# Optimization experiments

Measured on AMD Instinct MI355X. Metric: run time of the kernel, lower is better.

## Reference

```python
import jax, jax.numpy as jnp
import numpy as np

D_MODEL = 1024
NUM_HEADS = 16
HEAD_DIM = D_MODEL // NUM_HEADS
D_FF = 4096
BATCH = 4
SEQ = 2048
LN_EPS = 1e-6
NEG_INF = -1e10


def setup_inputs() -> dict:
    key = jax.random.key(0)
    ks = jax.random.split(key, 8)
    def lin_init(k, fan_in, fan_out):
        # flax default: lecun_normal kernel, zeros bias
        w = jax.random.normal(k, (fan_in, fan_out), jnp.float32) / np.sqrt(fan_in)
        b = jnp.zeros((fan_out,), jnp.float32)
        return w, b
    x = jax.random.normal(ks[0], (BATCH, SEQ, D_MODEL), jnp.float32)
    w_qkv, b_qkv = lin_init(ks[1], D_MODEL, 3 * D_MODEL)
    w_out, b_out = lin_init(ks[2], D_MODEL, D_MODEL)
    w_fc1, b_fc1 = lin_init(ks[3], D_MODEL, D_FF)
    w_fc2, b_fc2 = lin_init(ks[4], D_FF, D_MODEL)
    ln1_scale = jnp.ones((D_MODEL,), jnp.float32)
    ln1_bias = jnp.zeros((D_MODEL,), jnp.float32)
    ln2_scale = jnp.ones((D_MODEL,), jnp.float32)
    ln2_bias = jnp.zeros((D_MODEL,), jnp.float32)
    return {
        'x': x,
        'w_qkv': w_qkv, 'b_qkv': b_qkv,
        'w_out': w_out, 'b_out': b_out,
        'w_fc1': w_fc1, 'b_fc1': b_fc1,
        'w_fc2': w_fc2, 'b_fc2': b_fc2,
        'ln1_scale': ln1_scale, 'ln1_bias': ln1_bias,
        'ln2_scale': ln2_scale, 'ln2_bias': ln2_bias,
    }


def _layernorm(x, scale, bias):
    mu = jnp.mean(x, axis=-1, keepdims=True)
    var = jnp.mean(jnp.square(x - mu), axis=-1, keepdims=True)
    return (x - mu) * jax.lax.rsqrt(var + LN_EPS) * scale + bias


def _attention(x, w_qkv, b_qkv, w_out, b_out):
    B, S, _ = x.shape
    qkv = x @ w_qkv + b_qkv                      # [B,S,3*D]
    qkv = qkv.reshape(B, S, 3, NUM_HEADS, HEAD_DIM)
    q, k, v = qkv[:, :, 0], qkv[:, :, 1], qkv[:, :, 2]   # [B,S,H,D]
    q = q.transpose(0, 2, 1, 3)                  # [B,H,S,D]
    k = k.transpose(0, 2, 1, 3)
    v = v.transpose(0, 2, 1, 3)
    scores = jnp.einsum('bhqd,bhkd->bhqk', q, k) / np.sqrt(HEAD_DIM)
    causal = jnp.tril(jnp.ones((S, S), bool))[None, None]
    scores = jnp.where(causal, scores, NEG_INF)
    attn = jax.nn.softmax(scores, axis=-1)
    out = jnp.einsum('bhqk,bhkd->bhqd', attn, v)  # [B,H,S,D]
    out = out.transpose(0, 2, 1, 3).reshape(B, S, D_MODEL)
    return out @ w_out + b_out


def _mlp(x, w_fc1, b_fc1, w_fc2, b_fc2):
    h = jax.nn.gelu(x @ w_fc1 + b_fc1)  # approximate (tanh) gelu, matching nnx.gelu default
    return h @ w_fc2 + b_fc2


def reference(x, w_qkv, b_qkv, w_out, b_out, w_fc1, b_fc1, w_fc2, b_fc2,
              ln1_scale, ln1_bias, ln2_scale, ln2_bias):
    x = x + _attention(_layernorm(x, ln1_scale, ln1_bias), w_qkv, b_qkv, w_out, b_out)
    x = x + _mlp(_layernorm(x, ln2_scale, ln2_bias), w_fc1, b_fc1, w_fc2, b_fc2)
    return x
```

## Files before the change

kernel.cpp:

```cpp
#include <hip/hip_runtime.h>

typedef unsigned short u16;
typedef unsigned int u32;
typedef __bf16 bf16x8 __attribute__((ext_vector_type(8)));
typedef float f32x4 __attribute__((ext_vector_type(4)));

constexpr int SEQ = 2048;

__device__ __forceinline__ float bf2f(u16 u) {
    u32 x = ((u32)u) << 16;
    return __builtin_bit_cast(float, x);
}
__device__ __forceinline__ u16 f2bf(float f) {
    u32 u = __builtin_bit_cast(u32, f);
    u32 r = u + 0x7fffu + ((u >> 16) & 1u);
    return (u16)(r >> 16);
}
__device__ __forceinline__ bf16x8 ld_frag(const u16* p) {
    uint4 u = *(const uint4*)p;
    return __builtin_bit_cast(bf16x8, u);
}
__device__ __forceinline__ float gelu_f(float x) {
    float u = 0.7978845608028654f * (x + 0.044715f * x * x * x);
    float e = exp2f(u * 2.885390081777927f);
    float t = 1.f - 2.f / (1.f + e);
    return 0.5f * x * (1.f + t);
}
__device__ __forceinline__ bool probe_f32(const u32* p) { return (p[0] & 0xFFFFu) == 0u; }

__device__ __forceinline__ void load_lds16(const u16* g, u16* l) {
    __builtin_amdgcn_global_load_lds(
        (const __attribute__((address_space(1))) void*)g,
        (__attribute__((address_space(3))) void*)l, 16, 0, 0);
}

__global__ __launch_bounds__(256) void convert_to_bf16(const void* __restrict__ in, long long off,
                                                       u16* __restrict__ out, int n,
                                                       const u32* __restrict__ probe) {
    const bool f32 = probe_f32(probe);
    int i = (blockIdx.x * 256 + threadIdx.x) * 4;
    if (i >= n) return;
    if (f32) {
        const float4 v = *(const float4*)((const float*)in + off + i);
        uint2 o;
        o.x = (u32)f2bf(v.x) | ((u32)f2bf(v.y) << 16);
        o.y = (u32)f2bf(v.z) | ((u32)f2bf(v.w) << 16);
        *(uint2*)(out + i) = o;
    } else {
        *(uint2*)(out + i) = *(const uint2*)((const u16*)in + off + i);
    }
}

__global__ __launch_bounds__(256) void finalize_out(const u16* __restrict__ in, void* __restrict__ outv,
                                                    long long off, int n, const u32* __restrict__ probe) {
    const bool f32 = probe_f32(probe);
    int i = (blockIdx.x * 256 + threadIdx.x) * 4;
    if (i >= n) return;
    uint2 v = *(const uint2*)(in + i);
    if (f32) {
        float4 o;
        o.x = bf2f((u16)(v.x & 0xffffu));
        o.y = bf2f((u16)(v.x >> 16));
        o.z = bf2f((u16)(v.y & 0xffffu));
        o.w = bf2f((u16)(v.y >> 16));
        *(float4*)((float*)outv + off + i) = o;
    } else {
        *(uint2*)((u16*)outv + off + i) = v;
    }
}

__global__ __launch_bounds__(256) void transpose_any(const void* __restrict__ in,
                                                     u16* __restrict__ out,
                                                     int K, int N, const u32* __restrict__ probe) {
    const bool f32 = probe_f32(probe);
    __shared__ u16 tile[32][33];
    int tx = threadIdx.x & 31, ty = threadIdx.x >> 5;
    int k0 = blockIdx.y * 32, n0 = blockIdx.x * 32;
    for (int i = 0; i < 32; i += 8) {
        size_t idx = (size_t)(k0 + ty + i) * N + n0 + tx;
        tile[ty + i][tx] = f32 ? f2bf(((const float*)in)[idx]) : ((const u16*)in)[idx];
    }
    __syncthreads();
    for (int i = 0; i < 32; i += 8)
        out[(size_t)(n0 + ty + i) * K + k0 + tx] = tile[tx][ty + i];
}

__global__ __launch_bounds__(256) void layernorm_k(const u16* __restrict__ x,
                                                   const u16* __restrict__ sc,
                                                   const u16* __restrict__ bi,
                                                   u16* __restrict__ out) {
    int row = blockIdx.x;
    int tid = threadIdx.x;
    const u16* xr = x + (size_t)row * 1024;
    uint2 u = *(const uint2*)(xr + tid * 4);
    float v[4];
    v[0] = bf2f((u16)(u.x & 0xffffu));
    v[1] = bf2f((u16)(u.x >> 16));
    v[2] = bf2f((u16)(u.y & 0xffffu));
    v[3] = bf2f((u16)(u.y >> 16));
    float s1 = 0.f, s2 = 0.f;
    for (int i = 0; i < 4; i++) { s1 += v[i]; s2 += v[i] * v[i]; }
    for (int off = 32; off >= 1; off >>= 1) {
        s1 += __shfl_xor(s1, off, 64);
        s2 += __shfl_xor(s2, off, 64);
    }
    __shared__ float red[8];
    int wave = tid >> 6, lane = tid & 63;
    if (lane == 0) { red[wave] = s1; red[4 + wave] = s2; }
    __syncthreads();
    s1 = red[0] + red[1] + red[2] + red[3];
    s2 = red[4] + red[5] + red[6] + red[7];
    float mean = s1 * (1.f / 1024.f);
    float var = s2 * (1.f / 1024.f) - mean * mean;
    float rstd = rsqrtf(var + 1e-6f);
    u32 o0, o1;
    {
        int c = tid * 4;
        float y0 = (v[0] - mean) * rstd * bf2f(sc[c + 0]) + bf2f(bi[c + 0]);
        float y1 = (v[1] - mean) * rstd * bf2f(sc[c + 1]) + bf2f(bi[c + 1]);
        float y2 = (v[2] - mean) * rstd * bf2f(sc[c + 2]) + bf2f(bi[c + 2]);
        float y3 = (v[3] - mean) * rstd * bf2f(sc[c + 3]) + bf2f(bi[c + 3]);
        o0 = (u32)f2bf(y0) | ((u32)f2bf(y1) << 16);
        o1 = (u32)f2bf(y2) | ((u32)f2bf(y3) << 16);
    }
    uint2 ov; ov.x = o0; ov.y = o1;
    *(uint2*)(out + (size_t)row * 1024 + tid * 4) = ov;
}

__device__ __forceinline__ void gemm_core(const u16* __restrict__ A, const u16* __restrict__ Bt,
                                          int K, int bm, int bn,
                                          u16* lA, u16* lB, f32x4 acc[4][4]) {
    const int tid = threadIdx.x, lane = tid & 63, wave = tid >> 6;
    const int wr = (wave >> 1) * 64, wc = (wave & 1) * 64;
    const int g = lane >> 4, l15 = lane & 15;
    const int srow = wave * 32 + (lane >> 3);
    const int scol = (lane & 7) * 8;
    const u16* gA = A + (size_t)(bm + srow) * K + scol;
    const u16* gB = Bt + (size_t)(bn + srow) * K + scol;
    u16* lAb = lA + wave * 2048;
    u16* lBb = lB + wave * 2048;

    for (int kk = 0; kk < K; kk += 64) {
        __syncthreads();
#pragma unroll
        for (int q = 0; q < 4; q++) {
            load_lds16(gA + kk + q * 8 * K, lAb + q * 512);
            load_lds16(gB + kk + q * 8 * K, lBb + q * 512);
        }
        __syncthreads();
#pragma unroll
        for (int kh = 0; kh < 2; kh++) {
            bf16x8 af[4], bfr[4];
#pragma unroll
            for (int i = 0; i < 4; i++)
                af[i] = ld_frag(lA + (wr + i * 16 + l15) * 64 + (kh * 4 + g) * 8);
#pragma unroll
            for (int j = 0; j < 4; j++)
                bfr[j] = ld_frag(lB + (wc + j * 16 + l15) * 64 + (kh * 4 + g) * 8);
#pragma unroll
            for (int i = 0; i < 4; i++)
#pragma unroll
                for (int j = 0; j < 4; j++)
                    acc[i][j] = __builtin_amdgcn_mfma_f32_16x16x32_bf16(bfr[j], af[i], acc[i][j], 0, 0, 0);
        }
    }
}

__global__ __launch_bounds__(256) void gemm_bt(const u16* __restrict__ A,
                                               const u16* __restrict__ Bt,
                                               const u16* __restrict__ bias,
                                               const u16* __restrict__ res,
                                               u16* __restrict__ out,
                                               int M, int N, int K, int epi) {
    __shared__ __align__(16) u16 lA[128 * 64];
    __shared__ __align__(16) u16 lB[128 * 64];
    const int tid = threadIdx.x, lane = tid & 63, wave = tid >> 6;
    const int wr = (wave >> 1) * 64, wc = (wave & 1) * 64;
    const int g = lane >> 4, l15 = lane & 15;
    const int bm = blockIdx.y * 128, bn = blockIdx.x * 128;

    f32x4 acc[4][4];
    f32x4 zero = {0.f, 0.f, 0.f, 0.f};
    for (int i = 0; i < 4; i++)
        for (int j = 0; j < 4; j++) acc[i][j] = zero;

    gemm_core(A, Bt, K, bm, bn, lA, lB, acc);

    for (int j = 0; j < 4; j++) {
        const int gn0 = bn + wc + j * 16 + g * 4;
        const uint2 bv2 = *(const uint2*)(bias + gn0);
        const float b0 = bf2f((u16)(bv2.x & 0xffffu)), b1 = bf2f((u16)(bv2.x >> 16));
        const float b2 = bf2f((u16)(bv2.y & 0xffffu)), b3 = bf2f((u16)(bv2.y >> 16));
        for (int i = 0; i < 4; i++) {
            const int gm = bm + wr + i * 16 + l15;
            float v0 = acc[i][j][0] + b0, v1 = acc[i][j][1] + b1;
            float v2 = acc[i][j][2] + b2, v3 = acc[i][j][3] + b3;
            if (epi == 1) {
                const uint2 rv = *(const uint2*)(res + (size_t)gm * N + gn0);
                v0 += bf2f((u16)(rv.x & 0xffffu)); v1 += bf2f((u16)(rv.x >> 16));
                v2 += bf2f((u16)(rv.y & 0xffffu)); v3 += bf2f((u16)(rv.y >> 16));
            } else if (epi == 2) {
                v0 = gelu_f(v0); v1 = gelu_f(v1); v2 = gelu_f(v2); v3 = gelu_f(v3);
            }
            ushort4 o4;
            o4.x = f2bf(v0); o4.y = f2bf(v1); o4.z = f2bf(v2); o4.w = f2bf(v3);
            *(ushort4*)(out + (size_t)gm * N + gn0) = o4;
        }
    }
}

__global__ __launch_bounds__(256) void gemm_qkv(const u16* __restrict__ A,
                                                const u16* __restrict__ Bt,
                                                const u16* __restrict__ bias,
                                                u16* __restrict__ Qg,
                                                u16* __restrict__ Kg,
                                                u16* __restrict__ VTg,
                                                int K) {
    __shared__ __align__(16) u16 lA[128 * 64];
    __shared__ __align__(16) u16 lB[128 * 64];
    const int tid = threadIdx.x, lane = tid & 63, wave = tid >> 6;
    const int wr = (wave >> 1) * 64, wc = (wave & 1) * 64;
    const int g = lane >> 4, l15 = lane & 15;
    const int bm = blockIdx.y * 128, bn = blockIdx.x * 128;
    const float QSCALE = 0.18033688011112042f;

    f32x4 acc[4][4];
    f32x4 zero = {0.f, 0.f, 0.f, 0.f};
    for (int i = 0; i < 4; i++)
        for (int j = 0; j < 4; j++) acc[i][j] = zero;

    gemm_core(A, Bt, K, bm, bn, lA, lB, acc);

    for (int j = 0; j < 4; j++) {
        const int gn0 = bn + wc + j * 16 + g * 4;
        const int which = gn0 >> 10;
        const int hh = (gn0 >> 6) & 15, d0 = gn0 & 63;
        const uint2 bv2 = *(const uint2*)(bias + gn0);
        const float b0 = bf2f((u16)(bv2.x & 0xffffu)), b1 = bf2f((u16)(bv2.x >> 16));
        const float b2 = bf2f((u16)(bv2.y & 0xffffu)), b3 = bf2f((u16)(bv2.y >> 16));
        for (int i = 0; i < 4; i++) {
            const int s0 = bm + wr + i * 16 + l15;
            const int b = s0 >> 11, srel = s0 & 2047;
            const int bh = b * 16 + hh;
            const float v0 = acc[i][j][0] + b0, v1 = acc[i][j][1] + b1;
            const float v2 = acc[i][j][2] + b2, v3 = acc[i][j][3] + b3;
            if (which == 0) {
                ushort4 o4;
                o4.x = f2bf(v0 * QSCALE); o4.y = f2bf(v1 * QSCALE);
                o4.z = f2bf(v2 * QSCALE); o4.w = f2bf(v3 * QSCALE);
                *(ushort4*)(Qg + ((size_t)bh * SEQ + srel) * 64 + d0) = o4;
            } else if (which == 1) {
                ushort4 o4;
                o4.x = f2bf(v0); o4.y = f2bf(v1); o4.z = f2bf(v2); o4.w = f2bf(v3);
                *(ushort4*)(Kg + ((size_t)bh * SEQ + srel) * 64 + d0) = o4;
            } else {
                VTg[((size_t)bh * 64 + d0 + 0) * SEQ + srel] = f2bf(v0);
                VTg[((size_t)bh * 64 + d0 + 1) * SEQ + srel] = f2bf(v1);
                VTg[((size_t)bh * 64 + d0 + 2) * SEQ + srel] = f2bf(v2);
                VTg[((size_t)bh * 64 + d0 + 3) * SEQ + srel] = f2bf(v3);
            }
        }
    }
}

__device__ __forceinline__ void stage_kv(const u16* Kbh, const u16* Vbh, int kv0,
                                         u16* bK, u16* bV, int lane, int wave) {
    const int r = lane >> 3, c = (lane & 7) * 8;
#pragma unroll
    for (int q = 0; q < 2; q++) {
        const int row = q * 32 + wave * 8 + r;
        load_lds16(Kbh + (size_t)(kv0 + row) * 64 + c, bK + q * 2048 + wave * 512 + lane * 8);
        load_lds16(Vbh + (size_t)row * SEQ + kv0 + c, bV + q * 2048 + wave * 512 + lane * 8);
    }
}

__global__ __launch_bounds__(256) void flash_attn5(const u16* __restrict__ Qg,
                                                   const u16* __restrict__ Kg,
                                                   const u16* __restrict__ VTg,
                                                   u16* __restrict__ attn) {
    __shared__ __align__(16) u16 lK[2][64 * 64];
    __shared__ __align__(16) u16 lVt[2][64 * 64];
    __shared__ __align__(16) u16 lP[4 * 32 * 72];

    const int bh = blockIdx.y;
    const int tid = threadIdx.x, lane = tid & 63, wave = tid >> 6;
    const int g = lane >> 4, l15 = lane & 15;
    const float MASKV = -3.0e4f;

    const u16* Qbh = Qg + (size_t)bh * SEQ * 64;
    const u16* Kbh = Kg + (size_t)bh * SEQ * 64;
    const u16* Vbh = VTg + (size_t)bh * 64 * SEQ;
    u16* myP = lP + wave * 32 * 72;
    const int b = bh >> 4, h = bh & 15;
    const f32x4 zero = {0.f, 0.f, 0.f, 0.f};

    for (int ph = 0; ph < 2; ph++) {
        const int ti = ph ? blockIdx.x : (15 - blockIdx.x);
        const int q0 = ti * 128;
        const int qw = q0 + wave * 32;
        const int nfull = q0 >> 6;
        const int nt = nfull + 2;

        bf16x8 qf[2][2];
#pragma unroll
        for (int mi = 0; mi < 2; mi++)
#pragma unroll
            for (int kh = 0; kh < 2; kh++)
                qf[mi][kh] = ld_frag(Qbh + (size_t)(qw + mi * 16 + l15) * 64 + kh * 32 + g * 8);

        float l_[2][4];
        f32x4 o[2][4];
        for (int mi = 0; mi < 2; mi++)
            for (int r = 0; r < 4; r++) l_[mi][r] = 0.f;
        for (int mi = 0; mi < 2; mi++)
            for (int nj = 0; nj < 4; nj++) o[mi][nj] = zero;

        __syncthreads();
        stage_kv(Kbh, Vbh, 0, lK[0], lVt[0], lane, wave);

        for (int t = 0; t < nt; t++) {
            __syncthreads();
            if (t + 1 < nt)
                stage_kv(Kbh, Vbh, (t + 1) * 64, lK[(t + 1) & 1], lVt[(t + 1) & 1], lane, wave);
            const u16* bK = lK[t & 1];
            const u16* bV = lVt[t & 1];
            const bool diag = (t >= nfull);
            const int kv0 = t * 64;

            f32x4 sc[2][4];
#pragma unroll
            for (int mi = 0; mi < 2; mi++)
                for (int nj = 0; nj < 4; nj++) sc[mi][nj] = zero;
#pragma unroll
            for (int kh = 0; kh < 2; kh++) {
                bf16x8 kf[4];
#pragma unroll
                for (int nj = 0; nj < 4; nj++)
                    kf[nj] = ld_frag(bK + (nj * 16 + l15) * 64 + kh * 32 + g * 8);
#pragma unroll
                for (int mi = 0; mi < 2; mi++)
#pragma unroll
                    for (int nj = 0; nj < 4; nj++)
                        sc[mi][nj] = __builtin_amdgcn_mfma_f32_16x16x32_bf16(qf[mi][kh], kf[nj], sc[mi][nj], 0, 0, 0);
            }

#pragma unroll
            for (int mi = 0; mi < 2; mi++) {
#pragma unroll
                for (int r = 0; r < 4; r++) {
                    const int row = qw + mi * 16 + g * 4 + r;
                    float v0 = sc[mi][0][r], v1 = sc[mi][1][r];
                    float v2 = sc[mi][2][r], v3 = sc[mi][3][r];
                    if (diag) {
                        if (kv0 + 0 * 16 + l15 > row) v0 = MASKV;
                        if (kv0 + 1 * 16 + l15 > row) v1 = MASKV;
                        if (kv0 + 2 * 16 + l15 > row) v2 = MASKV;
                        if (kv0 + 3 * 16 + l15 > row) v3 = MASKV;
                    }
                    const float e0 = exp2f(v0), e1 = exp2f(v1);
                    const float e2 = exp2f(v2), e3 = exp2f(v3);
                    l_[mi][r] += (e0 + e1) + (e2 + e3);
                    const int prow = (mi * 16 + g * 4 + r) * 72;
                    myP[prow + 0 * 16 + l15] = f2bf(e0);
                    myP[prow + 1 * 16 + l15] = f2bf(e1);
                    myP[prow + 2 * 16 + l15] = f2bf(e2);
                    myP[prow + 3 * 16 + l15] = f2bf(e3);
                }
            }

#pragma unroll
            for (int ks = 0; ks < 2; ks++) {
                bf16x8 pa[2], vb[4];
#pragma unroll
                for (int mi = 0; mi < 2; mi++)
                    pa[mi] = ld_frag(myP + (mi * 16 + l15) * 72 + ks * 32 + g * 8);
#pragma unroll
                for (int nj = 0; nj < 4; nj++)
                    vb[nj] = ld_frag(bV + (nj * 16 + l15) * 64 + ks * 32 + g * 8);
#pragma unroll
                for (int mi = 0; mi < 2; mi++)
#pragma unroll
                    for (int nj = 0; nj < 4; nj++)
                        o[mi][nj] = __builtin_amdgcn_mfma_f32_16x16x32_bf16(pa[mi], vb[nj], o[mi][nj], 0, 0, 0);
            }
        }

#pragma unroll
        for (int mi = 0; mi < 2; mi++) {
            for (int r = 0; r < 4; r++) {
                float ls = l_[mi][r];
                for (int off = 1; off < 16; off <<= 1) ls += __shfl_xor(ls, off, 64);
                const float inv = 1.f / ls;
                const int row = qw + mi * 16 + g * 4 + r;
                const size_t orow = ((size_t)b * SEQ + row) * 1024 + h * 64;
                for (int nj = 0; nj < 4; nj++)
                    attn[orow + nj * 16 + l15] = f2bf(o[mi][nj][r] * inv);
            }
        }
    }
}

extern "C" void kernel_launch(void* const* d_in, const int* in_sizes, int n_in,
                              void* d_out, int out_size, void* d_ws, size_t ws_size,
                              hipStream_t stream) {
    const u32* probe = (const u32*)d_in[9];
    char* ws = (char*)d_ws;
    const size_t MB = 1048576;
    auto T = [&](size_t mb) { return (u16*)(ws + mb * MB); };
    auto conv = [&](const void* src, long long off, u16* dst, int n) {
        convert_to_bf16<<<(n / 4 + 255) / 256, 256, 0, stream>>>(src, off, dst, n, probe);
    };

    if (ws_size >= 160 * MB) {
        u16* xn1 = T(0), *Qg = T(16), *Kg = T(32), *VTg = T(48), *hbuf = T(0);
        u16* attn = T(64), *xn2 = T(64), *xbf = T(80), *resid1 = T(96), *outbf = T(112);
        u16* wTq = T(128), *wTo = T(134), *wT1 = T(136), *wT2 = T(144), *vecs = T(152);
        u16 *bqkvC = vecs, *boutC = vecs + 3072, *bfc1C = vecs + 4096, *bfc2C = vecs + 8192;
        u16 *ln1sC = vecs + 9216, *ln1bC = vecs + 10240, *ln2sC = vecs + 11264, *ln2bC = vecs + 12288;
        conv(d_in[2], 0, bqkvC, 3072); conv(d_in[4], 0, boutC, 1024);
        conv(d_in[6], 0, bfc1C, 4096); conv(d_in[8], 0, bfc2C, 1024);
        conv(d_in[9], 0, ln1sC, 1024); conv(d_in[10], 0, ln1bC, 1024);
        conv(d_in[11], 0, ln2sC, 1024); conv(d_in[12], 0, ln2bC, 1024);
        transpose_any<<<dim3(96, 32), 256, 0, stream>>>(d_in[1], wTq, 1024, 3072, probe);
        transpose_any<<<dim3(32, 32), 256, 0, stream>>>(d_in[3], wTo, 1024, 1024, probe);
        transpose_any<<<dim3(128, 32), 256, 0, stream>>>(d_in[5], wT1, 1024, 4096, probe);
        transpose_any<<<dim3(32, 128), 256, 0, stream>>>(d_in[7], wT2, 4096, 1024, probe);
        conv(d_in[0], 0, xbf, 8388608);
        layernorm_k<<<8192, 256, 0, stream>>>(xbf, ln1sC, ln1bC, xn1);
        gemm_qkv<<<dim3(24, 64), 256, 0, stream>>>(xn1, wTq, bqkvC, Qg, Kg, VTg, 1024);
        flash_attn5<<<dim3(8, 64), 256, 0, stream>>>(Qg, Kg, VTg, attn);
        gemm_bt<<<dim3(8, 64), 256, 0, stream>>>(attn, wTo, boutC, xbf, resid1, 8192, 1024, 1024, 1);
        layernorm_k<<<8192, 256, 0, stream>>>(resid1, ln2sC, ln2bC, xn2);
        gemm_bt<<<dim3(32, 64), 256, 0, stream>>>(xn2, wT1, bfc1C, nullptr, hbuf, 8192, 4096, 1024, 2);
        gemm_bt<<<dim3(8, 64), 256, 0, stream>>>(hbuf, wT2, bfc2C, resid1, outbf, 8192, 1024, 4096, 1);
        finalize_out<<<8192, 256, 0, stream>>>(outbf, d_out, 0, 8388608, probe);
    } else {
        u16* vecs = T(0);
        u16 *bqkvC = vecs, *boutC = vecs + 3072, *bfc1C = vecs + 4096, *bfc2C = vecs + 8192;
        u16 *ln1sC = vecs + 9216, *ln1bC = vecs + 10240, *ln2sC = vecs + 11264, *ln2bC = vecs + 12288;
        u16* wTq = T(1), *wTo = T(7), *wT1 = T(9), *wT2 = T(17);
        u16* xbf = T(25), *xn = T(29), *Qg = T(33), *Kg = T(37), *VTg = T(41);
        u16* attn_b = T(45), *resid_b = T(49), *h_b = T(53);
        conv(d_in[2], 0, bqkvC, 3072); conv(d_in[4], 0, boutC, 1024);
        conv(d_in[6], 0, bfc1C, 4096); conv(d_in[8], 0, bfc2C, 1024);
        conv(d_in[9], 0, ln1sC, 1024); conv(d_in[10], 0, ln1bC, 1024);
        conv(d_in[11], 0, ln2sC, 1024); conv(d_in[12], 0, ln2bC, 1024);
        transpose_any<<<dim3(96, 32), 256, 0, stream>>>(d_in[1], wTq, 1024, 3072, probe);
        transpose_any<<<dim3(32, 32), 256, 0, stream>>>(d_in[3], wTo, 1024, 1024, probe);
        transpose_any<<<dim3(128, 32), 256, 0, stream>>>(d_in[5], wT1, 1024, 4096, probe);
        transpose_any<<<dim3(32, 128), 256, 0, stream>>>(d_in[7], wT2, 4096, 1024, probe);
        for (int b = 0; b < 4; b++) {
            const long long ro = (long long)b * 2048 * 1024;
            conv(d_in[0], ro, xbf, 2097152);
            layernorm_k<<<2048, 256, 0, stream>>>(xbf, ln1sC, ln1bC, xn);
            gemm_qkv<<<dim3(24, 16), 256, 0, stream>>>(xn, wTq, bqkvC, Qg, Kg, VTg, 1024);
            flash_attn5<<<dim3(8, 16), 256, 0, stream>>>(Qg, Kg, VTg, attn_b);
            gemm_bt<<<dim3(8, 16), 256, 0, stream>>>(attn_b, wTo, boutC, xbf, resid_b, 2048, 1024, 1024, 1);
            layernorm_k<<<2048, 256, 0, stream>>>(resid_b, ln2sC, ln2bC, xn);
            for (int c = 0; c < 2; c++) {
                u16* xnc = xn + (size_t)c * 1024 * 1024;
                u16* resc = resid_b + (size_t)c * 1024 * 1024;
                u16* outc = xbf + (size_t)c * 1024 * 1024;
                gemm_bt<<<dim3(32, 8), 256, 0, stream>>>(xnc, wT1, bfc1C, nullptr, h_b, 1024, 4096, 1024, 2);
                gemm_bt<<<dim3(8, 8), 256, 0, stream>>>(h_b, wT2, bfc2C, resc, outc, 1024, 1024, 4096, 1);
                finalize_out<<<1024, 256, 0, stream>>>(outc, d_out, ro + c * 1048576, 1048576, probe);
            }
        }
    }
}
```

Measured before the change: 636.6 us.

## XOR-swizzle LDS tiles in GEMM and flash attention; fuse input convert with LayerNorm

Global-to-LDS loads now place each 16-byte chunk at a slot XORed with the row index, and fragment reads apply the matching XOR. This affects the GEMM core and the K/V staging in flash attention and is meant to remove LDS bank conflicts on the 64-wide bf16 rows. Separately, the input fp32-to-bf16 conversion and the first LayerNorm are merged into one kernel that writes both the bf16 copy and the normalized output, saving one pass over x. The swizzle has to match exactly between writer and reader; the visible hunks look consistent, but any other consumer of the same LDS buffers that was not updated would read wrong data.

```diff
diff --git a/kernel.cpp b/kernel.cpp
--- a/kernel.cpp
+++ b/kernel.cpp
@@ -83,6 +83,56 @@
     __syncthreads();
     for (int i = 0; i < 32; i += 8)
         out[(size_t)(n0 + ty + i) * K + k0 + tx] = tile[tx][ty + i];
+}
+
+__global__ __launch_bounds__(256) void fused_cvt_ln(const void* __restrict__ xraw, long long off,
+                                                    const u16* __restrict__ sc,
+                                                    const u16* __restrict__ bi,
+                                                    u16* __restrict__ xbf,
+                                                    u16* __restrict__ xn,
+                                                    const u32* __restrict__ probe) {
+    const bool f32 = probe_f32(probe);
+    int row = blockIdx.x;
+    int tid = threadIdx.x;
+    float v[4];
+    if (f32) {
+        const float4 q = *(const float4*)((const float*)xraw + off + (size_t)row * 1024 + tid * 4);
+        v[0] = q.x; v[1] = q.y; v[2] = q.z; v[3] = q.w;
+    } else {
+        uint2 u = *(const uint2*)((const u16*)xraw + off + (size_t)row * 1024 + tid * 4);
+        v[0] = bf2f((u16)(u.x & 0xffffu)); v[1] = bf2f((u16)(u.x >> 16));
+        v[2] = bf2f((u16)(u.y & 0xffffu)); v[3] = bf2f((u16)(u.y >> 16));
+    }
+    {
+        uint2 c;
+        c.x = (u32)f2bf(v[0]) | ((u32)f2bf(v[1]) << 16);
+        c.y = (u32)f2bf(v[2]) | ((u32)f2bf(v[3]) << 16);
+        *(uint2*)(xbf + (size_t)row * 1024 + tid * 4) = c;
+    }
+    float s1 = 0.f, s2 = 0.f;
+    for (int i = 0; i < 4; i++) { s1 += v[i]; s2 += v[i] * v[i]; }
+    for (int off2 = 32; off2 >= 1; off2 >>= 1) {
+        s1 += __shfl_xor(s1, off2, 64);
+        s2 += __shfl_xor(s2, off2, 64);
+    }
+    __shared__ float red[8];
+    int wave = tid >> 6, lane = tid & 63;
+    if (lane == 0) { red[wave] = s1; red[4 + wave] = s2; }
+    __syncthreads();
+    s1 = red[0] + red[1] + red[2] + red[3];
+    s2 = red[4] + red[5] + red[6] + red[7];
+    float mean = s1 * (1.f / 1024.f);
+    float var = s2 * (1.f / 1024.f) - mean * mean;
+    float rstd = rsqrtf(var + 1e-6f);
+    int c = tid * 4;
+    float y0 = (v[0] - mean) * rstd * bf2f(sc[c + 0]) + bf2f(bi[c + 0]);
+    float y1 = (v[1] - mean) * rstd * bf2f(sc[c + 1]) + bf2f(bi[c + 1]);
+    float y2 = (v[2] - mean) * rstd * bf2f(sc[c + 2]) + bf2f(bi[c + 2]);
+    float y3 = (v[3] - mean) * rstd * bf2f(sc[c + 3]) + bf2f(bi[c + 3]);
+    uint2 ov;
+    ov.x = (u32)f2bf(y0) | ((u32)f2bf(y1) << 16);
+    ov.y = (u32)f2bf(y2) | ((u32)f2bf(y3) << 16);
+    *(uint2*)(xn + (size_t)row * 1024 + tid * 4) = ov;
 }
 
 __global__ __launch_bounds__(256) void layernorm_k(const u16* __restrict__ x,
@@ -134,11 +184,12 @@
     const int wr = (wave >> 1) * 64, wc = (wave & 1) * 64;
     const int g = lane >> 4, l15 = lane & 15;
     const int srow = wave * 32 + (lane >> 3);
-    const int scol = (lane & 7) * 8;
-    const u16* gA = A + (size_t)(bm + srow) * K + scol;
-    const u16* gB = Bt + (size_t)(bn + srow) * K + scol;
+    const int gslot = (lane & 7) ^ (lane >> 3);
+    const u16* gA = A + (size_t)(bm + srow) * K + gslot * 8;
+    const u16* gB = Bt + (size_t)(bn + srow) * K + gslot * 8;
     u16* lAb = lA + wave * 2048;
     u16* lBb = lB + wave * 2048;
+    const int sw = (l15 & 7);
 
     for (int kk = 0; kk < K; kk += 64) {
         __syncthreads();
@@ -153,10 +204,10 @@
             bf16x8 af[4], bfr[4];
 #pragma unroll
             for (int i = 0; i < 4; i++)
-                af[i] = ld_frag(lA + (wr + i * 16 + l15) * 64 + (kh * 4 + g) * 8);
+                af[i] = ld_frag(lA + (wr + i * 16 + l15) * 64 + (((kh * 4 + g) ^ sw) * 8));
 #pragma unroll
             for (int j = 0; j < 4; j++)
-                bfr[j] = ld_frag(lB + (wc + j * 16 + l15) * 64 + (kh * 4 + g) * 8);
+                bfr[j] = ld_frag(lB + (wc + j * 16 + l15) * 64 + (((kh * 4 + g) ^ sw) * 8));
 #pragma unroll
             for (int i = 0; i < 4; i++)
 #pragma unroll
@@ -265,16 +316,17 @@
 
 __device__ __forceinline__ void stage_kv(const u16* Kbh, const u16* Vbh, int kv0,
                                          u16* bK, u16* bV, int lane, int wave) {
-    const int r = lane >> 3, c = (lane & 7) * 8;
+    const int r = lane >> 3;
+    const int gs = ((lane & 7) ^ r) * 8;
 #pragma unroll
     for (int q = 0; q < 2; q++) {
         const int row = q * 32 + wave * 8 + r;
-        load_lds16(Kbh + (size_t)(kv0 + row) * 64 + c, bK + q * 2048 + wave * 512 + lane * 8);
-        load_lds16(Vbh + (size_t)row * SEQ + kv0 + c, bV + q * 2048 + wave * 512 + lane * 8);
-    }
-}
-
-__global__ __launch_bounds__(256) void flash_attn5(const u16* __restrict__ Qg,
+        load_lds16(Kbh + (size_t)(kv0 + row) * 64 + gs, bK + q * 2048 + wave * 512 + lane * 8);
+        load_lds16(Vbh + (size_t)row * SEQ + kv0 + gs, bV + q * 2048 + wave * 512 + lane * 8);
+    }
+}
+
+__global__ __launch_bounds__(256) void flash_attn6(const u16* __restrict__ Qg,
                                                    const u16* __restrict__ Kg,
                                                    const u16* __restrict__ VTg,
                                                    u16* __restrict__ attn) {
@@ -293,6 +345,7 @@
     u16* myP = lP + wave * 32 * 72;
     const int b = bh >> 4, h = bh & 15;
     const f32x4 zero = {0.f, 0.f, 0.f, 0.f};
+    const int sw = (l15 & 7);
 
     for (int ph = 0; ph < 2; ph++) {
         const int ti = ph ? blockIdx.x : (15 - blockIdx.x);
@@ -336,7 +389,7 @@
                 bf16x8 kf[4];
 #pragma unroll
                 for (int nj = 0; nj < 4; nj++)
-                    kf[nj] = ld_frag(bK + (nj * 16 + l15) * 64 + kh * 32 + g * 8);
+                    kf[nj] = ld_frag(bK + (nj * 16 + l15) * 64 + (((kh * 4 + g) ^ sw) * 8));
 #pragma unroll
                 for (int mi = 0; mi < 2; mi++)
 #pragma unroll
@@ -376,7 +429,7 @@
                     pa[mi] = ld_frag(myP + (mi * 16 + l15) * 72 + ks * 32 + g * 8);
 #pragma unroll
                 for (int nj = 0; nj < 4; nj++)
-                    vb[nj] = ld_frag(bV + (nj * 16 + l15) * 64 + ks * 32 + g * 8);
+                    vb[nj] = ld_frag(bV + (nj * 16 + l15) * 64 + (((ks * 4 + g) ^ sw) * 8));
 #pragma unroll
                 for (int mi = 0; mi < 2; mi++)
 #pragma unroll
@@ -425,10 +478,9 @@
         transpose_any<<<dim3(32, 32), 256, 0, stream>>>(d_in[3], wTo, 1024, 1024, probe);
         transpose_any<<<dim3(128, 32), 256, 0, stream>>>(d_in[5], wT1, 1024, 4096, probe);
         transpose_any<<<dim3(32, 128), 256, 0, stream>>>(d_in[7], wT2, 4096, 1024, probe);
-        conv(d_in[0], 0, xbf, 8388608);
-        layernorm_k<<<8192, 256, 0, stream>>>(xbf, ln1sC, ln1bC, xn1);
+        fused_cvt_ln<<<8192, 256, 0, stream>>>(d_in[0], 0, ln1sC, ln1bC, xbf, xn1, probe);
         gemm_qkv<<<dim3(24, 64), 256, 0, stream>>>(xn1, wTq, bqkvC, Qg, Kg, VTg, 1024);
-        flash_attn5<<<dim3(8, 64), 256, 0, stream>>>(Qg, Kg, VTg, attn);
+        flash_attn6<<<dim3(8, 64), 256, 0, stream>>>(Qg, Kg, VTg, attn);
         gemm_bt<<<dim3(8, 64), 256, 0, stream>>>(attn, wTo, boutC, xbf, resid1, 8192, 1024, 1024, 1);
         layernorm_k<<<8192, 256, 0, stream>>>(resid1, ln2sC, ln2bC, xn2);
         gemm_bt<<<dim3(32, 64), 256, 0, stream>>>(xn2, wT1, bfc1C, nullptr, hbuf, 8192, 4096, 1024, 2);
@@ -451,10 +503,9 @@
         transpose_any<<<dim3(32, 128), 256, 0, stream>>>(d_in[7], wT2, 4096, 1024, probe);
         for (int b = 0; b < 4; b++) {
             const long long ro = (long long)b * 2048 * 1024;
-            conv(d_in[0], ro, xbf, 2097152);
-            layernorm_k<<<2048, 256, 0, stream>>>(xbf, ln1sC, ln1bC, xn);
+            fused_cvt_ln<<<2048, 256, 0, stream>>>(d_in[0], ro, ln1sC, ln1bC, xbf, xn, probe);
             gemm_qkv<<<dim3(24, 16), 256, 0, stream>>>(xn, wTq, bqkvC, Qg, Kg, VTg, 1024);
-            flash_attn5<<<dim3(8, 16), 256, 0, stream>>>(Qg, Kg, VTg, attn_b);
+            flash_attn6<<<dim3(8, 16), 256, 0, stream>>>(Qg, Kg, VTg, attn_b);
             gemm_bt<<<dim3(8, 16), 256, 0, stream>>>(attn_b, wTo, boutC, xbf, resid_b, 2048, 1024, 1024, 1);
             layernorm_k<<<2048, 256, 0, stream>>>(resid_b, ln2sC, ln2bC, xn);
             for (int c = 0; c < 2; c++) {
```

Result: faster. 575.0 us (-9.7%).
